# Optimization experiments

Measured on AMD Instinct MI355X. Metric: run time of the kernel, lower is better.

The kernel has to match this reference:

```python
import jax, jax.numpy as jnp
import numpy as np

D = 512
H = 8
HD = D // H
EPS = 1e-8


def setup_inputs() -> dict:
    key = jax.random.key(0)
    ks = jax.random.split(key, 16)
    B, S = 4, 2048
    s = lambda n: 1.0 / np.sqrt(n)
    inp = {
        "gene_emb": jax.random.normal(ks[0], (B, S, D), jnp.float32),
        "expr_emb": jax.random.normal(ks[1], (B, S, D), jnp.float32),
        "M": jax.random.uniform(ks[2], (B, S, S), jnp.float32),
        # weights stored (in, out) so y = x @ W + b
        "W_fused": jax.random.normal(ks[3], (2 * D, D), jnp.float32) * s(2 * D),
        "b_fused": jnp.zeros((D,), jnp.float32),
        "W_Q": jax.random.normal(ks[4], (D, D), jnp.float32) * s(D),
        "b_Q": jnp.zeros((D,), jnp.float32),
        "W_K": jax.random.normal(ks[5], (D, D), jnp.float32) * s(D),
        "b_K": jnp.zeros((D,), jnp.float32),
        "W_V": jax.random.normal(ks[6], (D, D), jnp.float32) * s(D),
        "b_V": jnp.zeros((D,), jnp.float32),
        "W_O": jax.random.normal(ks[7], (D, D), jnp.float32) * s(D),
        "b_O": jnp.zeros((D,), jnp.float32),
    }
    return inp


def reference(gene_emb, expr_emb, M, W_fused, b_fused, W_Q, b_Q, W_K, b_K, W_V, b_V, W_O, b_O):
    B, S, _ = gene_emb.shape
    scale = HD ** (-0.5)
    fused = jnp.concatenate([gene_emb, expr_emb], axis=-1) @ W_fused + b_fused
    # (B,S,D) -> (B,H,S,HD)
    split = lambda x: x.reshape(B, S, H, HD).transpose(0, 2, 1, 3)
    Q = split(fused @ W_Q + b_Q)
    K = split(fused @ W_K + b_K)
    V = split(expr_emb @ W_V + b_V)
    scores = jnp.einsum("bhqd,bhkd->bhqk", Q, K) * scale
    Mg = M[:, None, :, :]  # broadcast over heads
    scores = scores * Mg
    attn = jax.nn.softmax(scores, axis=-1)
    A_sparse = attn * Mg
    norm = jnp.sum(jnp.abs(A_sparse), axis=-1, keepdims=True) + EPS
    A_bar = A_sparse / norm
    out = jnp.einsum("bhqk,bhkd->bhqd", A_bar, V)
    out = out.transpose(0, 2, 1, 3).reshape(B, S, D)
    return out @ W_O + b_O
```

## Files before the change

### kernel.cpp

```cpp
#include <hip/hip_runtime.h>

typedef unsigned short u16;
typedef __attribute__((ext_vector_type(8))) short bf16x8_t;
typedef __attribute__((ext_vector_type(4))) float f32x4_t;
typedef __attribute__((ext_vector_type(16))) float f32x16_t;

__device__ __forceinline__ u16 f2bf(float x){
  union { float f; unsigned u; } v; v.f = x;
  unsigned r = v.u + 0x7FFFu + ((v.u >> 16) & 1u);
  return (u16)(r >> 16);
}
__device__ __forceinline__ float bf2f(u16 h){
  union { unsigned u; float f; } v; v.u = ((unsigned)h) << 16;
  return v.f;
}
__device__ __forceinline__ unsigned pack_hi16(float a, float b){
  union { float f; unsigned u; } x, y; x.f = a; y.f = b;
  return (x.u >> 16) | (y.u & 0xFFFF0000u);
}

__device__ __forceinline__ void gl2lds16(const u16* g, u16* l){
  __builtin_amdgcn_global_load_lds((const __attribute__((address_space(1))) void*)g,
                                   (__attribute__((address_space(3))) void*)l, 16, 0, 0);
}

__global__ __launch_bounds__(256) void split_concat_kernel(
    const float* __restrict__ gene, const float* __restrict__ expr,
    u16* __restrict__ Xh, u16* __restrict__ Xl)
{
  size_t e = ((size_t)blockIdx.x * 256 + threadIdx.x) * 4;
  int row = (int)(e >> 10);
  int col = (int)(e & 1023);
  const float* src = (col < 512) ? (gene + (size_t)row * 512 + col)
                                 : (expr + (size_t)row * 512 + (col - 512));
  float4 v = *(const float4*)src;
  float a[4] = {v.x, v.y, v.z, v.w};
  u16 hs[4], ls[4];
#pragma unroll
  for (int i = 0; i < 4; i++){
    hs[i] = f2bf(a[i]);
    ls[i] = f2bf(a[i] - bf2f(hs[i]));
  }
  *(uint2*)(Xh + e) = make_uint2(hs[0] | ((unsigned)hs[1] << 16), hs[2] | ((unsigned)hs[3] << 16));
  *(uint2*)(Xl + e) = make_uint2(ls[0] | ((unsigned)ls[1] << 16), ls[2] | ((unsigned)ls[3] << 16));
}

__global__ __launch_bounds__(256) void transpose_all_kernel(
    const float* __restrict__ Wf, const float* __restrict__ Wq,
    const float* __restrict__ Wk, const float* __restrict__ Wv,
    const float* __restrict__ Wo,
    u16* __restrict__ Wfth, u16* __restrict__ Wftl,
    u16* __restrict__ Wqth, u16* __restrict__ Wkth,
    u16* __restrict__ Wvth, u16* __restrict__ Woth)
{
  __shared__ float t[64][65];
  int id = blockIdx.x;
  const float* W; u16* Th; u16* Tl; int K, kx, ny;
  if (id < 128){ W = Wf; Th = Wfth; Tl = Wftl; K = 1024; kx = id >> 3; ny = id & 7; }
  else {
    int tt = id - 128; int wi = tt >> 6; tt &= 63; kx = tt >> 3; ny = tt & 7; K = 512;
    W  = (wi == 0) ? Wq  : (wi == 1) ? Wk  : (wi == 2) ? Wv  : Wo;
    Th = (wi == 0) ? Wqth: (wi == 1) ? Wkth: (wi == 2) ? Wvth: Woth;
    Tl = nullptr;
  }
  int k0 = kx * 64, n0 = ny * 64;
  int tid = threadIdx.x;
  int r = tid >> 4;
  int c4 = (tid & 15) * 4;
#pragma unroll
  for (int p = 0; p < 4; p++){
    int k = p * 16 + r;
    float4 v = *(const float4*)(W + (size_t)(k0 + k) * 512 + n0 + c4);
    t[c4 + 0][k] = v.x; t[c4 + 1][k] = v.y; t[c4 + 2][k] = v.z; t[c4 + 3][k] = v.w;
  }
  __syncthreads();
#pragma unroll
  for (int p = 0; p < 4; p++){
    int n = p * 16 + r;
    u16 hs[4], ls[4];
#pragma unroll
    for (int i = 0; i < 4; i++){
      float x = t[n][c4 + i];
      hs[i] = f2bf(x);
      ls[i] = f2bf(x - bf2f(hs[i]));
    }
    size_t o = (size_t)(n0 + n) * K + k0 + c4;
    *(uint2*)(Th + o) = make_uint2(hs[0] | ((unsigned)hs[1] << 16), hs[2] | ((unsigned)hs[3] << 16));
    if (Tl)
      *(uint2*)(Tl + o) = make_uint2(ls[0] | ((unsigned)ls[1] << 16), ls[2] | ((unsigned)ls[3] << 16));
  }
}

template<int SPLITS, int MODE, int DUAL>
__global__ __launch_bounds__(256, 2) void gemm_kernel(
    const u16* __restrict__ Ah, const u16* __restrict__ Al, int lda,
    const u16* __restrict__ Bh0, const u16* __restrict__ Bl0,
    const u16* __restrict__ Bh1, int K,
    const float* __restrict__ bias0, const float* __restrict__ bias1,
    void* __restrict__ out0, void* __restrict__ out1, void* __restrict__ outsec,
    float sc0, float sc1)
{
  __shared__ __align__(16) u16 sAh[128 * 32];
  __shared__ __align__(16) u16 sAl[SPLITS >= 2 ? 128 * 32 : 8];
  __shared__ __align__(16) u16 sBh[64 * 32];
  __shared__ __align__(16) u16 sBl[SPLITS == 3 ? 64 * 32 : 8];
  int tid = threadIdx.x;
  int lane = tid & 63, w = tid >> 6, quad = lane >> 4, l15 = lane & 15;
  int wm = w & 1, wn = w >> 1;
  int m0 = blockIdx.x * 128;
  int side = DUAL ? (int)(blockIdx.y >> 3) : 0;
  int n0 = (DUAL ? (int)(blockIdx.y & 7) : (int)blockIdx.y) * 64;
  const u16* Bh = (DUAL && side) ? Bh1 : Bh0;
  const float* bias = (DUAL && side) ? bias1 : bias0;
  void* o0 = (DUAL && side) ? outsec : out0;
  float sc = (DUAL && side) ? sc1 : sc0;

  f32x4_t acc[4][2];
#pragma unroll
  for (int i = 0; i < 4; i++)
#pragma unroll
    for (int j = 0; j < 2; j++)
#pragma unroll
      for (int r = 0; r < 4; r++) acc[i][j][r] = 0.f;

  int lrow = lane >> 2;
  int swzS = ((lane >> 2) & 3) ^ ((lane >> 4) & 3);
  int gkq  = ((lane & 3) ^ swzS) * 8;
  const u16* pAh0 = Ah + (size_t)(m0 + w * 32 + lrow) * lda + gkq;
  const u16* pAh1 = Ah + (size_t)(m0 + w * 32 + 16 + lrow) * lda + gkq;
  const u16* pAl0 = (SPLITS >= 2) ? Al + (size_t)(m0 + w * 32 + lrow) * lda + gkq : nullptr;
  const u16* pAl1 = (SPLITS >= 2) ? Al + (size_t)(m0 + w * 32 + 16 + lrow) * lda + gkq : nullptr;
  const u16* pBh0 = Bh + (size_t)(n0 + w * 16 + lrow) * K + gkq;
  const u16* pBl0 = (SPLITS == 3) ? Bl0 + (size_t)(n0 + w * 16 + lrow) * K + gkq : nullptr;
  u16* dAh = sAh + w * 1024;
  u16* dAl = sAl + w * 1024;
  u16* dBh = sBh + w * 512;
  u16* dBl = sBl + w * 512;

  int pq = (quad ^ ((l15 & 3) ^ ((l15 >> 2) & 3))) * 8;

  for (int k0 = 0; k0 < K; k0 += 32){
    __syncthreads();
    gl2lds16(pAh0 + k0, dAh);
    gl2lds16(pAh1 + k0, dAh + 512);
    if constexpr (SPLITS >= 2){
      gl2lds16(pAl0 + k0, dAl);
      gl2lds16(pAl1 + k0, dAl + 512);
    }
    gl2lds16(pBh0 + k0, dBh);
    if constexpr (SPLITS == 3)
      gl2lds16(pBl0 + k0, dBl);
    __syncthreads();

    bf16x8_t aH[4], aL[4], bH[2], bL[2];
#pragma unroll
    for (int mi = 0; mi < 4; mi++){
      int ad = (wm * 64 + mi * 16 + l15) * 32 + pq;
      aH[mi] = *(const bf16x8_t*)&sAh[ad];
      if constexpr (SPLITS >= 2) aL[mi] = *(const bf16x8_t*)&sAl[ad];
    }
#pragma unroll
    for (int ni = 0; ni < 2; ni++){
      int bd = (wn * 32 + ni * 16 + l15) * 32 + pq;
      bH[ni] = *(const bf16x8_t*)&sBh[bd];
      if constexpr (SPLITS == 3) bL[ni] = *(const bf16x8_t*)&sBl[bd];
    }
#pragma unroll
    for (int mi = 0; mi < 4; mi++)
#pragma unroll
      for (int ni = 0; ni < 2; ni++){
        acc[mi][ni] = __builtin_amdgcn_mfma_f32_16x16x32_bf16(aH[mi], bH[ni], acc[mi][ni], 0, 0, 0);
        if constexpr (SPLITS == 3)
          acc[mi][ni] = __builtin_amdgcn_mfma_f32_16x16x32_bf16(aH[mi], bL[ni], acc[mi][ni], 0, 0, 0);
        if constexpr (SPLITS >= 2)
          acc[mi][ni] = __builtin_amdgcn_mfma_f32_16x16x32_bf16(aL[mi], bH[ni], acc[mi][ni], 0, 0, 0);
      }
  }

#pragma unroll
  for (int mi = 0; mi < 4; mi++)
#pragma unroll
    for (int ni = 0; ni < 2; ni++){
      int gn = n0 + wn * 32 + ni * 16 + l15;
      float bs = bias[gn];
      int gm0 = m0 + wm * 64 + mi * 16 + quad * 4;
#pragma unroll
      for (int r = 0; r < 4; r++){
        float v = acc[mi][ni][r] + bs;
        int gm = gm0 + r;
        if constexpr (MODE == 0){
          u16 hb = f2bf(v);
          ((u16*)o0)[(size_t)gm * 512 + gn] = hb;
          ((u16*)out1)[(size_t)gm * 512 + gn] = f2bf(v - bf2f(hb));
        } else if constexpr (MODE == 1){
          ((u16*)o0)[(size_t)gm * 512 + gn] = f2bf(v * sc);
        } else if constexpr (MODE == 2){
          int bb = gm >> 11, s = gm & 2047;
          int hh = gn >> 6, d = gn & 63;
          ((u16*)o0)[((size_t)((bb * 8 + hh) * 64 + d) << 11) + s] = f2bf(v);
        } else {
          ((float*)o0)[(size_t)gm * 512 + gn] = v;
        }
      }
    }
}

__global__ __launch_bounds__(256, 2) void flash_kernel(
    const u16* __restrict__ Qh, const u16* __restrict__ Kh,
    const u16* __restrict__ Vt, const float* __restrict__ Mm,
    u16* __restrict__ Oh)
{
  __shared__ __align__(16) u16 sAll[2][16384];
  int tid = threadIdx.x, lane = tid & 63, w = tid >> 6;
  int ql = lane & 31, hi = lane >> 5;
  int wq = w >> 1, wk = w & 1;
  int by = blockIdx.y, b = by >> 2, h0 = (by & 3) * 2;
  int q0 = blockIdx.x * 64;
  int q  = q0 + wq * 32 + ql;

  const u16* qp = Qh + ((size_t)(b * 2048 + q)) * 512 + h0 * 64 + hi * 8;
  bf16x8_t qf[2][4];
#pragma unroll
  for (int h = 0; h < 2; h++)
#pragma unroll
    for (int dt = 0; dt < 4; dt++)
      qf[h][dt] = *(const bf16x8_t*)(qp + h * 64 + dt * 16);

  int srow = lane >> 3, c8 = lane & 7;
  const u16* gK[4]; const u16* gV[4];
#pragma unroll
  for (int c = 0; c < 4; c++){
    int kv = wk * 32 + c * 8 + srow;
    int skey = ((c >> 1) << 2) | ((c & 1) << 1) | (srow & 1);
    gK[c] = Kh + ((size_t)(b * 2048 + kv)) * 512 + (h0 + wq) * 64 + ((c8 ^ skey) << 3);
    gV[c] = Vt + ((size_t)((b * 8 + h0 + wq) * 64 + kv)) * 2048 + ((c8 ^ srow) << 3);
  }
  int dO = wq * 4096 + wk * 2048;

  int phi = ((ql >> 3) & 1) * 16 + ((ql >> 2) & 1) * 8 + (ql >> 4) * 4 + (ql & 3);
  int kvL = wk * 32 + phi;
  int skr = ((ql >> 3) & 1) * 4 + ((ql >> 2) & 1) * 2 + (ql & 1);
  int kaddr[4];
#pragma unroll
  for (int dt = 0; dt < 4; dt++)
    kaddr[dt] = kvL * 64 + (((dt * 2 + hi) ^ skr) << 3);
  int vaddr[2][2];
#pragma unroll
  for (int dn = 0; dn < 2; dn++)
#pragma unroll
    for (int kt = 0; kt < 2; kt++)
      vaddr[dn][kt] = (dn * 32 + ql) * 64 + (((wk * 4 + kt * 2 + hi) ^ (ql & 7)) << 3);

  const float* mp = Mm + (size_t)b * (2048 * 2048) + (size_t)q * 2048 + wk * 32 + hi * 8;
  const int og[4] = {0, 16, 4, 20};

  float lp[2] = {0.f, 0.f};
  f32x16_t Oc[2][2];
#pragma unroll
  for (int h = 0; h < 2; h++)
#pragma unroll
    for (int dn = 0; dn < 2; dn++)
#pragma unroll
      for (int r = 0; r < 16; r++) Oc[h][dn][r] = 0.f;

#define STAGE(B, KK) do {                                              \
    _Pragma("unroll")                                                  \
    for (int c = 0; c < 4; c++){                                       \
      gl2lds16(gK[c] + (size_t)(KK) * 512, &sAll[B][dO + c * 512]);    \
      gl2lds16(gV[c] + (KK),               &sAll[B][8192 + dO + c * 512]); \
    }                                                                  \
  } while (0)

  STAGE(0, 0);
  f32x4_t Mc[4], Mn[4];
#pragma unroll
  for (int g = 0; g < 4; g++) Mc[g] = *(const f32x4_t*)(mp + og[g]);
  __syncthreads();

  for (int t = 0; t < 32; ++t){
    int ph = t & 1;
    bool nx = t < 31;
    if (nx) STAGE(ph ^ 1, (t + 1) * 64);
    if (nx){
#pragma unroll
      for (int g = 0; g < 4; g++) Mn[g] = *(const f32x4_t*)(mp + (t + 1) * 64 + og[g]);
    }
    const u16* kb = &sAll[ph][0];
    const u16* vb = &sAll[ph][8192];

#pragma unroll
    for (int h = 0; h < 2; ++h){
      const u16* kbh = kb + h * 4096;
      const u16* vbh = vb + h * 4096;

      f32x16_t S;
#pragma unroll
      for (int r = 0; r < 16; r++) S[r] = 0.f;
#pragma unroll
      for (int dt = 0; dt < 4; dt++){
        bf16x8_t kf = *(const bf16x8_t*)&kbh[kaddr[dt]];
        S = __builtin_amdgcn_mfma_f32_32x32x16_bf16(kf, qf[h][dt], S, 0, 0, 0);
      }

      float p[16];
#pragma unroll
      for (int g = 0; g < 4; g++)
#pragma unroll
        for (int e = 0; e < 4; e++){
          float m = Mc[g][e];
          float v = m * __builtin_amdgcn_exp2f(S[g * 4 + e] * m);
          lp[h] += v;
          p[g * 4 + e] = v;
        }
#pragma unroll
      for (int kt = 0; kt < 2; kt++){
        union { unsigned u[4]; bf16x8_t v8; } pb;
        pb.u[0] = pack_hi16(p[kt * 4 + 0], p[kt * 4 + 1]);
        pb.u[1] = pack_hi16(p[kt * 4 + 2], p[kt * 4 + 3]);
        pb.u[2] = pack_hi16(p[kt * 4 + 8], p[kt * 4 + 9]);
        pb.u[3] = pack_hi16(p[kt * 4 + 10], p[kt * 4 + 11]);
#pragma unroll
        for (int dn = 0; dn < 2; dn++){
          bf16x8_t vf = *(const bf16x8_t*)&vbh[vaddr[dn][kt]];
          Oc[h][dn] = __builtin_amdgcn_mfma_f32_32x32x16_bf16(vf, pb.v8, Oc[h][dn], 0, 0, 0);
        }
      }
    }

    __syncthreads();
    if (nx){
#pragma unroll
      for (int g = 0; g < 4; g++) Mc[g] = Mn[g];
    }
  }
#undef STAGE

  lp[0] += __shfl_xor(lp[0], 32);
  lp[1] += __shfl_xor(lp[1], 32);

  float* red = (float*)&sAll[0][0];
  float* lpr = red + 8192;
  if (wk){
#pragma unroll
    for (int h = 0; h < 2; h++){
#pragma unroll
      for (int dn = 0; dn < 2; dn++)
#pragma unroll
        for (int rq = 0; rq < 4; rq++){
          f32x4_t o;
          o[0] = Oc[h][dn][rq * 4 + 0]; o[1] = Oc[h][dn][rq * 4 + 1];
          o[2] = Oc[h][dn][rq * 4 + 2]; o[3] = Oc[h][dn][rq * 4 + 3];
          *(f32x4_t*)&red[((((wq * 2 + h) * 2 + dn) * 4 + rq) * 64 + lane) * 4] = o;
        }
      lpr[(wq * 2 + h) * 64 + lane] = lp[h];
    }
  }
  __syncthreads();
  if (!wk){
#pragma unroll
    for (int h = 0; h < 2; h++){
      float li = lp[h] + lpr[(wq * 2 + h) * 64 + lane];
      float inv = 1.0f / li;
      size_t ob = ((size_t)(b * 2048 + q)) * 512 + (h0 + h) * 64;
#pragma unroll
      for (int dn = 0; dn < 2; dn++)
#pragma unroll
        for (int rq = 0; rq < 4; rq++){
          f32x4_t o = *(const f32x4_t*)&red[((((wq * 2 + h) * 2 + dn) * 4 + rq) * 64 + lane) * 4];
          float v0 = (Oc[h][dn][rq * 4 + 0] + o[0]) * inv;
          float v1 = (Oc[h][dn][rq * 4 + 1] + o[1]) * inv;
          float v2 = (Oc[h][dn][rq * 4 + 2] + o[2]) * inv;
          float v3 = (Oc[h][dn][rq * 4 + 3] + o[3]) * inv;
          int d0 = dn * 32 + rq * 8 + hi * 4;
          unsigned w0 = (unsigned)f2bf(v0) | ((unsigned)f2bf(v1) << 16);
          unsigned w1 = (unsigned)f2bf(v2) | ((unsigned)f2bf(v3) << 16);
          *(uint2*)(Oh + ob + d0) = make_uint2(w0, w1);
        }
    }
  }
}

extern "C" void kernel_launch(void* const* d_in, const int* in_sizes, int n_in,
                              void* d_out, int out_size, void* d_ws, size_t ws_size,
                              hipStream_t stream)
{
  const float* gene = (const float*)d_in[0];
  const float* expr = (const float*)d_in[1];
  const float* Mm   = (const float*)d_in[2];
  const float* Wf   = (const float*)d_in[3];
  const float* bfv  = (const float*)d_in[4];
  const float* Wq   = (const float*)d_in[5];
  const float* bq   = (const float*)d_in[6];
  const float* Wk   = (const float*)d_in[7];
  const float* bk   = (const float*)d_in[8];
  const float* Wv   = (const float*)d_in[9];
  const float* bv   = (const float*)d_in[10];
  const float* Wo   = (const float*)d_in[11];
  const float* bo   = (const float*)d_in[12];
  float* out = (float*)d_out;

  char* ws = (char*)d_ws;
  size_t off = 0;
  auto alloc = [&](size_t bytes) -> void* {
    void* p = (void*)(ws + off);
    off += (bytes + 255) & ~(size_t)255;
    return p;
  };
  u16* Xh   = (u16*)alloc(8192ull * 1024 * 2);
  u16* Xl   = (u16*)alloc(8192ull * 1024 * 2);
  u16* Wfth = (u16*)alloc(512ull * 1024 * 2);
  u16* Wftl = (u16*)alloc(512ull * 1024 * 2);
  u16* Wqth = (u16*)alloc(512ull * 512 * 2);
  u16* Wkth = (u16*)alloc(512ull * 512 * 2);
  u16* Wvth = (u16*)alloc(512ull * 512 * 2);
  u16* Woth = (u16*)alloc(512ull * 512 * 2);
  u16* Fh   = (u16*)alloc(8192ull * 512 * 2);
  u16* Fl   = (u16*)alloc(8192ull * 512 * 2);
  u16* Qh   = (u16*)alloc(8192ull * 512 * 2);
  u16* Kh   = (u16*)alloc(8192ull * 512 * 2);
  u16* Vt   = (u16*)alloc(8192ull * 512 * 2);
  u16* Oh = Xh;

  const float QSC = 0.1803368801f;

  split_concat_kernel<<<8192, 256, 0, stream>>>(gene, expr, Xh, Xl);
  transpose_all_kernel<<<384, 256, 0, stream>>>(Wf, Wq, Wk, Wv, Wo,
                                                Wfth, Wftl, Wqth, Wkth, Wvth, Woth);

  gemm_kernel<3, 0, 0><<<dim3(64, 8), 256, 0, stream>>>(
      Xh, Xl, 1024, Wfth, Wftl, nullptr, 1024, bfv, nullptr, Fh, Fl, nullptr, 1.f, 1.f);
  gemm_kernel<2, 1, 1><<<dim3(64, 16), 256, 0, stream>>>(
      Fh, Fl, 512, Wqth, nullptr, Wkth, 512, bq, bk, Qh, nullptr, Kh, QSC, 1.f);
  gemm_kernel<2, 2, 0><<<dim3(64, 8), 256, 0, stream>>>(
      Xh + 512, Xl + 512, 1024, Wvth, nullptr, nullptr, 512, bv, nullptr, Vt, nullptr, nullptr, 1.f, 1.f);
  flash_kernel<<<dim3(32, 16), 256, 0, stream>>>(Qh, Kh, Vt, Mm, Oh);
  gemm_kernel<1, 3, 0><<<dim3(64, 8), 256, 0, stream>>>(
      Oh, nullptr, 512, Woth, nullptr, nullptr, 512, bo, nullptr, out, nullptr, nullptr, 1.f, 1.f);

  (void)in_sizes; (void)n_in; (void)out_size; (void)ws_size;
}
```

Measured before the change: 301.7 us.

## Unroll attention loop by two with explicit vmcnt waits and priority hints

Restructures the double-buffered attention main loop into a two-phase unrolled form with static buffer indices and ping-pong mask registers. It replaces __syncthreads with an explicit s_waitcnt vmcnt(4) plus s_barrier fenced by sched_barrier, so the next tile's async LDS loads can stay in flight across the barrier. It also raises wave priority around the MFMA sections and packs bf16 pairs with a single v_perm. The hand-counted vmcnt relies on the exact ordering of the LDS-direct loads against the mask loads, which is fragile if the compiler reorders them.

```diff
diff --git a/kernel.cpp b/kernel.cpp
--- a/kernel.cpp
+++ b/kernel.cpp
@@ -17,6 +17,10 @@
 __device__ __forceinline__ unsigned pack_hi16(float a, float b){
   union { float f; unsigned u; } x, y; x.f = a; y.f = b;
   return (x.u >> 16) | (y.u & 0xFFFF0000u);
+}
+__device__ __forceinline__ unsigned packp(float a, float b){
+  union { float f; unsigned u; } x, y; x.f = a; y.f = b;
+  return __builtin_amdgcn_perm(y.u, x.u, 0x07060302u);
 }
 
 __device__ __forceinline__ void gl2lds16(const u16* g, u16* l){
@@ -271,69 +275,95 @@
     }                                                                  \
   } while (0)
 
+#define COMPUTE(PH, MARR) do {                                          \
+    const u16* kb_ = &sAll[PH][0];                                      \
+    const u16* vb_ = &sAll[PH][8192];                                   \
+    _Pragma("unroll")                                                   \
+    for (int h = 0; h < 2; ++h){                                        \
+      const u16* kbh = kb_ + h * 4096;                                  \
+      const u16* vbh = vb_ + h * 4096;                                  \
+      f32x16_t S;                                                       \
+      _Pragma("unroll")                                                 \
+      for (int r = 0; r < 16; r++) S[r] = 0.f;                          \
+      __builtin_amdgcn_s_setprio(1);                                    \
+      _Pragma("unroll")                                                 \
+      for (int dt = 0; dt < 4; dt++){                                   \
+        bf16x8_t kf = *(const bf16x8_t*)&kbh[kaddr[dt]];                \
+        S = __builtin_amdgcn_mfma_f32_32x32x16_bf16(kf, qf[h][dt], S, 0, 0, 0); \
+      }                                                                 \
+      __builtin_amdgcn_s_setprio(0);                                    \
+      float p[16];                                                      \
+      _Pragma("unroll")                                                 \
+      for (int g = 0; g < 4; g++)                                       \
+        _Pragma("unroll")                                               \
+        for (int e = 0; e < 4; e++){                                    \
+          float m = MARR[g][e];                                         \
+          float v = m * __builtin_amdgcn_exp2f(S[g * 4 + e] * m);       \
+          lp[h] += v;                                                   \
+          p[g * 4 + e] = v;                                             \
+        }                                                               \
+      __builtin_amdgcn_s_setprio(1);                                    \
+      _Pragma("unroll")                                                 \
+      for (int kt = 0; kt < 2; kt++){                                   \
+        union { unsigned u[4]; bf16x8_t v8; } pb;                       \
+        pb.u[0] = packp(p[kt * 4 + 0], p[kt * 4 + 1]);                  \
+        pb.u[1] = packp(p[kt * 4 + 2], p[kt * 4 + 3]);                  \
+        pb.u[2] = packp(p[kt * 4 + 8], p[kt * 4 + 9]);                  \
+        pb.u[3] = packp(p[kt * 4 + 10], p[kt * 4 + 11]);                \
+        _Pragma("unroll")                                               \
+        for (int dn = 0; dn < 2; dn++){                                 \
+          bf16x8_t vf = *(const bf16x8_t*)&vbh[vaddr[dn][kt]];          \
+          Oc[h][dn] = __builtin_amdgcn_mfma_f32_32x32x16_bf16(vf, pb.v8, Oc[h][dn], 0, 0, 0); \
+        }                                                               \
+      }                                                                 \
+      __builtin_amdgcn_s_setprio(0);                                    \
+    }                                                                   \
+  } while (0)
+
+#define FENCE_BARRIER() do {                                            \
+    __builtin_amdgcn_sched_barrier(0);                                  \
+    __builtin_amdgcn_s_barrier();                                       \
+    __builtin_amdgcn_sched_barrier(0);                                  \
+  } while (0)
+
+  f32x4_t MA[4], MB[4];
+
   STAGE(0, 0);
-  f32x4_t Mc[4], Mn[4];
-#pragma unroll
-  for (int g = 0; g < 4; g++) Mc[g] = *(const f32x4_t*)(mp + og[g]);
-  __syncthreads();
-
-  for (int t = 0; t < 32; ++t){
-    int ph = t & 1;
-    bool nx = t < 31;
-    if (nx) STAGE(ph ^ 1, (t + 1) * 64);
-    if (nx){
-#pragma unroll
-      for (int g = 0; g < 4; g++) Mn[g] = *(const f32x4_t*)(mp + (t + 1) * 64 + og[g]);
-    }
-    const u16* kb = &sAll[ph][0];
-    const u16* vb = &sAll[ph][8192];
-
-#pragma unroll
-    for (int h = 0; h < 2; ++h){
-      const u16* kbh = kb + h * 4096;
-      const u16* vbh = vb + h * 4096;
-
-      f32x16_t S;
-#pragma unroll
-      for (int r = 0; r < 16; r++) S[r] = 0.f;
-#pragma unroll
-      for (int dt = 0; dt < 4; dt++){
-        bf16x8_t kf = *(const bf16x8_t*)&kbh[kaddr[dt]];
-        S = __builtin_amdgcn_mfma_f32_32x32x16_bf16(kf, qf[h][dt], S, 0, 0, 0);
+  __builtin_amdgcn_sched_barrier(0);
+#pragma unroll
+  for (int g = 0; g < 4; g++) MA[g] = *(const f32x4_t*)(mp + og[g]);
+  asm volatile("s_waitcnt vmcnt(4)" ::: "memory");
+  FENCE_BARRIER();
+
+  for (int tt = 0; tt < 16; ++tt){
+    {
+      int t = tt * 2;
+      STAGE(1, (t + 1) * 64);
+      __builtin_amdgcn_sched_barrier(0);
+#pragma unroll
+      for (int g = 0; g < 4; g++) MB[g] = *(const f32x4_t*)(mp + (t + 1) * 64 + og[g]);
+      COMPUTE(0, MA);
+      asm volatile("s_waitcnt vmcnt(4)" ::: "memory");
+      FENCE_BARRIER();
+    }
+    {
+      int t = tt * 2 + 1;
+      bool nx = t < 31;
+      if (nx){
+        STAGE(0, (t + 1) * 64);
+        __builtin_amdgcn_sched_barrier(0);
+#pragma unroll
+        for (int g = 0; g < 4; g++) MA[g] = *(const f32x4_t*)(mp + (t + 1) * 64 + og[g]);
       }
-
-      float p[16];
-#pragma unroll
-      for (int g = 0; g < 4; g++)
-#pragma unroll
-        for (int e = 0; e < 4; e++){
-          float m = Mc[g][e];
-          float v = m * __builtin_amdgcn_exp2f(S[g * 4 + e] * m);
-          lp[h] += v;
-          p[g * 4 + e] = v;
-        }
-#pragma unroll
-      for (int kt = 0; kt < 2; kt++){
-        union { unsigned u[4]; bf16x8_t v8; } pb;
-        pb.u[0] = pack_hi16(p[kt * 4 + 0], p[kt * 4 + 1]);
-        pb.u[1] = pack_hi16(p[kt * 4 + 2], p[kt * 4 + 3]);
-        pb.u[2] = pack_hi16(p[kt * 4 + 8], p[kt * 4 + 9]);
-        pb.u[3] = pack_hi16(p[kt * 4 + 10], p[kt * 4 + 11]);
-#pragma unroll
-        for (int dn = 0; dn < 2; dn++){
-          bf16x8_t vf = *(const bf16x8_t*)&vbh[vaddr[dn][kt]];
-          Oc[h][dn] = __builtin_amdgcn_mfma_f32_32x32x16_bf16(vf, pb.v8, Oc[h][dn], 0, 0, 0);
-        }
-      }
-    }
-
-    __syncthreads();
-    if (nx){
-#pragma unroll
-      for (int g = 0; g < 4; g++) Mc[g] = Mn[g];
+      COMPUTE(1, MB);
+      if (nx) asm volatile("s_waitcnt vmcnt(4)" ::: "memory");
+      else    asm volatile("s_waitcnt vmcnt(0)" ::: "memory");
+      FENCE_BARRIER();
     }
   }
 #undef STAGE
+#undef COMPUTE
+#undef FENCE_BARRIER
 
   lp[0] += __shfl_xor(lp[0], 32);
   lp[1] += __shfl_xor(lp[1], 32);
```

Result: slower. 368.0 us (+21.9%).
